# Optimization experiments

Hardware: AMD Instinct MI355X
Metric: run time of the kernel (lower is better)

The kernel has to match this reference:

```python
import jax, jax.numpy as jnp
import numpy as np

L, C, H, DH, S, N, B = 12, 768, 12, 64, 2, 577, 1
ALT_START, ROPE_START = 0, 0
OUT_LAYERS = (2, 5, 8, 11)
EPS = 1e-6


def _ln(x, w, b):
    m = jnp.mean(x, axis=-1, keepdims=True)
    v = jnp.var(x, axis=-1, keepdims=True)
    return (x - m) * jax.lax.rsqrt(v + EPS) * w + b


def _rms(x, w):
    return x * jax.lax.rsqrt(jnp.mean(x * x, axis=-1, keepdims=True) + EPS) * w


def _rot_half(x):
    h = x.shape[-1] // 2
    return jnp.concatenate([-x[..., h:], x[..., :h]], axis=-1)


def _rope(t, cos, sin):
    # t: [Bf, H, N, DH]; cos/sin: [N, DH] split into y/x halves
    h = t.shape[-1] // 2
    tv, th = t[..., :h], t[..., h:]
    cy, cx = cos[..., :h], cos[..., h:]
    sy, sx = sin[..., :h], sin[..., h:]
    return jnp.concatenate([tv * cy + _rot_half(tv) * sy,
                            th * cx + _rot_half(th) * sx], axis=-1)


def _block(xf, cos, sin, kv, p):
    (qkv_w, qkv_b, qn, kn, pw, pb, g1, g2,
     n1w, n1b, n2w, n2b, f1w, f1b, f2w, f2b) = p
    Bf, Nn, Cc = xf.shape
    h = _ln(xf, n1w, n1b)
    qkv = (jnp.einsum('bnc,oc->bno', h, qkv_w) + qkv_b)
    qkv = qkv.reshape(Bf, Nn, 3, H, DH).transpose(2, 0, 3, 1, 4)
    q, k, v = qkv[0], qkv[1], qkv[2]
    q, k = _rms(q, qn), _rms(k, kn)
    q, k = _rope(q, cos, sin), _rope(k, cos, sin)
    bias = ((1.0 - kv) * (-10000.0))[:, None, None, :]
    scores = jnp.einsum('bhqd,bhkd->bhqk', q, k) / np.sqrt(DH) + bias
    attn = jax.nn.softmax(scores, axis=-1)
    o = jnp.einsum('bhqk,bhkd->bhqd', attn, v).transpose(0, 2, 1, 3).reshape(Bf, Nn, Cc)
    o = jnp.einsum('bnc,oc->bno', o, pw) + pb
    xf = xf + g1 * o
    h2 = _ln(xf, n2w, n2b)
    m = jax.nn.gelu(jnp.einsum('bnc,oc->bno', h2, f1w) + f1b, approximate=False)
    m = jnp.einsum('bnd,od->bno', m, f2w) + f2b
    return xf + g2 * m


def _forward(x, rope_cos_local, rope_sin_local, rope_cos_global, rope_sin_global,
             key_valid_local, key_valid_global, camera_token,
             qkv_w, qkv_b, q_norm_w, k_norm_w, proj_w, proj_b,
             ls1_gamma, ls2_gamma, norm1_w, norm1_b, norm2_w, norm2_b,
             fc1_w, fc1_b, fc2_w, fc2_b, final_norm_w, final_norm_b):
    Bb, Ss, Nn, Cc = x.shape
    stacked = (qkv_w, qkv_b, q_norm_w, k_norm_w, proj_w, proj_b, ls1_gamma,
               ls2_gamma, norm1_w, norm1_b, norm2_w, norm2_b, fc1_w, fc1_b,
               fc2_w, fc2_b)
    local_x = x
    outputs = []
    cam_token_out = None
    max_out = max(OUT_LAYERS)
    for i in range(L):
        if i == ALT_START:
            ref = jnp.broadcast_to(camera_token[:, :1], (Bb, 1, Cc))
            src = jnp.broadcast_to(camera_token[:, 1:], (Bb, Ss - 1, Cc))
            x = x.at[:, :, 0].set(jnp.concatenate([ref, src], axis=1))
        p = tuple(a[i] for a in stacked)
        is_global = (i % 2 == 1)  # alt_start == 0
        if is_global:
            xf = x.reshape(Bb, Ss * Nn, Cc)
            xf = _block(xf, rope_cos_global, rope_sin_global, key_valid_global, p)
            x = xf.reshape(Bb, Ss, Nn, Cc)
        else:
            xf = x.reshape(Bb * Ss, Nn, Cc)
            xf = _block(xf, rope_cos_local, rope_sin_local, key_valid_local, p)
            x = xf.reshape(Bb, Ss, Nn, Cc)
            local_x = x
        if i in OUT_LAYERS:
            out_x = jnp.concatenate([local_x, x], axis=-1)  # cat_token=True
            outputs.append(out_x)
            if i == max_out:
                cam_token_out = out_x[:, :, 0]
    processed = []
    for o in outputs:
        o = jnp.concatenate([o[..., :Cc], _ln(o[..., Cc:], final_norm_w, final_norm_b)], axis=-1)
        o = o[..., 1:, :]  # drop cam/cls token (num_register_tokens=0)
        processed.append(o)
    return (processed[0], processed[1], processed[2], processed[3], cam_token_out)


def setup_inputs() -> dict:
    key = jax.random.key(0)
    ks = iter(jax.random.split(key, 40))
    rn = lambda sh, s=0.02: jax.random.normal(next(ks), sh, dtype=jnp.float32) * s
    two_pi = 2.0 * np.pi
    ang_l = jax.random.uniform(next(ks), (N, DH), dtype=jnp.float32) * two_pi
    ang_g = jax.random.uniform(next(ks), (S * N, DH), dtype=jnp.float32) * two_pi
    kv_l = (jax.random.uniform(next(ks), (B * S, N)) > 0.1).astype(jnp.float32)
    kv_g = (jax.random.uniform(next(ks), (B, S * N)) > 0.1).astype(jnp.float32)
    return {
        'x': rn((B, S, N, C), 1.0),
        'rope_cos_local': jnp.cos(ang_l), 'rope_sin_local': jnp.sin(ang_l),
        'rope_cos_global': jnp.cos(ang_g), 'rope_sin_global': jnp.sin(ang_g),
        'key_valid_local': kv_l, 'key_valid_global': kv_g,
        'camera_token': rn((1, 2, C)),
        'qkv_w': rn((L, 3 * C, C)), 'qkv_b': rn((L, 3 * C)),
        'q_norm_w': jnp.ones((L, DH), jnp.float32),
        'k_norm_w': jnp.ones((L, DH), jnp.float32),
        'proj_w': rn((L, C, C)), 'proj_b': rn((L, C)),
        'ls1_gamma': rn((L, C), 0.1), 'ls2_gamma': rn((L, C), 0.1),
        'norm1_w': jnp.ones((L, C), jnp.float32), 'norm1_b': jnp.zeros((L, C), jnp.float32),
        'norm2_w': jnp.ones((L, C), jnp.float32), 'norm2_b': jnp.zeros((L, C), jnp.float32),
        'fc1_w': rn((L, 4 * C, C)), 'fc1_b': rn((L, 4 * C)),
        'fc2_w': rn((L, C, 4 * C)), 'fc2_b': rn((L, C)),
        'final_norm_w': jnp.ones((C,), jnp.float32),
        'final_norm_b': jnp.zeros((C,), jnp.float32),
    }


def reference(x, rope_cos_local, rope_sin_local, rope_cos_global, rope_sin_global,
              key_valid_local, key_valid_global, camera_token,
              qkv_w, qkv_b, q_norm_w, k_norm_w, proj_w, proj_b,
              ls1_gamma, ls2_gamma, norm1_w, norm1_b, norm2_w, norm2_b,
              fc1_w, fc1_b, fc2_w, fc2_b, final_norm_w, final_norm_b):
    return _forward(x, rope_cos_local, rope_sin_local, rope_cos_global, rope_sin_global,
                    key_valid_local, key_valid_global, camera_token,
                    qkv_w, qkv_b, q_norm_w, k_norm_w, proj_w, proj_b,
                    ls1_gamma, ls2_gamma, norm1_w, norm1_b, norm2_w, norm2_b,
                    fc1_w, fc1_b, fc2_w, fc2_b, final_norm_w, final_norm_b)
```

## Files before the change

### kernel.cpp

```cpp
#include <hip/hip_runtime.h>
#include <hip/hip_bf16.h>
#include <math.h>

typedef __hip_bfloat16 bf16;
typedef __attribute__((ext_vector_type(4))) float floatx4;
typedef __attribute__((ext_vector_type(8))) short shortx8;

#define T_TOK 1154
#define C_DIM 768
#define H_HEADS 12
#define NLOC 577
#define OUT_PER 1769472

#define NQ  1769472ull
#define NP  589824ull
#define NF1 2359296ull
#define NF2 2359296ull
#define NWTOT 7077888ull
#define WQ  0ull
#define WP  1769472ull
#define WF1 2359296ull
#define WF2 4718592ull

static __device__ __forceinline__ float b2f(bf16 v) { return __bfloat162float(v); }
static __device__ __forceinline__ bf16 f2b(float v) { return __float2bfloat16(v); }

__global__ void k_init(const float* __restrict__ xin, const float* __restrict__ cam,
                       float* __restrict__ xF, int total) {
    int idx = blockIdx.x * 256 + threadIdx.x;
    if (idx >= total) return;
    int t = idx / C_DIM, c = idx - t * C_DIM;
    int s = t / NLOC, n = t - s * NLOC;
    float v = (n == 0) ? cam[s * C_DIM + c] : xin[idx];
    xF[idx] = v;
}

__global__ void k_cast(const float* __restrict__ src, bf16* __restrict__ dst, int total) {
    int idx = blockIdx.x * 256 + threadIdx.x;
    if (idx < total) dst[idx] = f2b(src[idx]);
}

__global__ __launch_bounds__(256) void k_wconv(
    const float* __restrict__ wq, const float* __restrict__ wp,
    const float* __restrict__ wf1, const float* __restrict__ wf2,
    bf16* __restrict__ dst) {
    size_t e = ((size_t)blockIdx.x * 256 + threadIdx.x) * 8;
    if (e >= NWTOT) return;
    const float* src; size_t off;
    if (e < WP)       { src = wq;  off = e; }
    else if (e < WF1) { src = wp;  off = e - WP; }
    else if (e < WF2) { src = wf1; off = e - WF1; }
    else              { src = wf2; off = e - WF2; }
    float4 a = *(const float4*)(src + off);
    float4 b = *(const float4*)(src + off + 4);
    bf16 pk[8];
    pk[0] = f2b(a.x); pk[1] = f2b(a.y); pk[2] = f2b(a.z); pk[3] = f2b(a.w);
    pk[4] = f2b(b.x); pk[5] = f2b(b.y); pk[6] = f2b(b.z); pk[7] = f2b(b.w);
    *(shortx8*)(dst + e) = *(shortx8*)pk;
}

__global__ __launch_bounds__(256) void k_ln(const float* __restrict__ xF,
                                            const float* __restrict__ w, const float* __restrict__ b,
                                            bf16* __restrict__ out) {
    int t = blockIdx.x;
    const float* xr = xF + (size_t)t * C_DIM;
    float s = 0.f, s2 = 0.f;
    for (int c = threadIdx.x; c < C_DIM; c += 256) { float v = xr[c]; s += v; s2 += v * v; }
    __shared__ float red[8];
    for (int o = 32; o; o >>= 1) { s += __shfl_xor(s, o, 64); s2 += __shfl_xor(s2, o, 64); }
    int wv = threadIdx.x >> 6;
    if ((threadIdx.x & 63) == 0) { red[wv] = s; red[4 + wv] = s2; }
    __syncthreads();
    s = red[0] + red[1] + red[2] + red[3];
    s2 = red[4] + red[5] + red[6] + red[7];
    float mean = s * (1.0f / C_DIM);
    float var = s2 * (1.0f / C_DIM) - mean * mean;
    if (var < 0.f) var = 0.f;
    float inv = rsqrtf(var + 1e-6f);
    bf16* orow = out + (size_t)t * C_DIM;
    for (int c = threadIdx.x; c < C_DIM; c += 256) {
        float v = (xr[c] - mean) * inv * w[c] + b[c];
        orow[c] = f2b(v);
    }
}

__global__ __launch_bounds__(256) void k_gemm(
    const bf16* __restrict__ A, const bf16* __restrict__ Bt,
    const float* __restrict__ bias, const float* __restrict__ gamma,
    bf16* __restrict__ outB, float* __restrict__ xio,
    int M, int N, int K, int mB, int mode) {
    __shared__ short At[64 * 72];
    __shared__ short Bs[64 * 72];
    int nwg = gridDim.x;
    int lid = blockIdx.x;
    int qd = nwg >> 3, rm = nwg & 7;
    int xcd = lid & 7, pos = lid >> 3;
    int lid2 = (xcd < rm ? xcd * (qd + 1) : rm * (qd + 1) + (xcd - rm) * qd) + pos;
    int mI = lid2 % mB, nI = lid2 / mB;
    int m0 = mI * 64, n0 = nI * 64;
    int tid = threadIdx.x;
    int wv = tid >> 6, lane = tid & 63;
    int mt = (wv & 1) * 32, nt = (wv >> 1) * 32;
    floatx4 acc[2][2] = {};
    int r = tid >> 2, cS = (tid & 3) * 16;
    int arow = m0 + r; if (arow >= M) arow = M - 1;
    const bf16* aptr = A + (size_t)arow * K + cS;
    const bf16* bptr = Bt + (size_t)(n0 + r) * K + cS;
    short* asl = &At[r * 72 + cS];
    short* bsl = &Bs[r * 72 + cS];
    int lrow = lane & 15, lq = lane >> 4;
    const short* aRd = &At[(mt + lrow) * 72 + lq * 8];
    const short* bRd = &Bs[(nt + lrow) * 72 + lq * 8];
    for (int k0 = 0; k0 < K; k0 += 64) {
        *(uint4*)asl       = *(const uint4*)(aptr);
        *(uint4*)(asl + 8) = *(const uint4*)(aptr + 8);
        *(uint4*)bsl       = *(const uint4*)(bptr);
        *(uint4*)(bsl + 8) = *(const uint4*)(bptr + 8);
        aptr += 64; bptr += 64;
        __syncthreads();
        shortx8 a00 = *(const shortx8*)(aRd);
        shortx8 a10 = *(const shortx8*)(aRd + 16 * 72);
        shortx8 b00 = *(const shortx8*)(bRd);
        shortx8 b10 = *(const shortx8*)(bRd + 16 * 72);
        shortx8 a01 = *(const shortx8*)(aRd + 32);
        shortx8 a11 = *(const shortx8*)(aRd + 16 * 72 + 32);
        shortx8 b01 = *(const shortx8*)(bRd + 32);
        shortx8 b11 = *(const shortx8*)(bRd + 16 * 72 + 32);
        acc[0][0] = __builtin_amdgcn_mfma_f32_16x16x32_bf16(a00, b00, acc[0][0], 0, 0, 0);
        acc[0][1] = __builtin_amdgcn_mfma_f32_16x16x32_bf16(a00, b10, acc[0][1], 0, 0, 0);
        acc[1][0] = __builtin_amdgcn_mfma_f32_16x16x32_bf16(a10, b00, acc[1][0], 0, 0, 0);
        acc[1][1] = __builtin_amdgcn_mfma_f32_16x16x32_bf16(a10, b10, acc[1][1], 0, 0, 0);
        acc[0][0] = __builtin_amdgcn_mfma_f32_16x16x32_bf16(a01, b01, acc[0][0], 0, 0, 0);
        acc[0][1] = __builtin_amdgcn_mfma_f32_16x16x32_bf16(a01, b11, acc[0][1], 0, 0, 0);
        acc[1][0] = __builtin_amdgcn_mfma_f32_16x16x32_bf16(a11, b01, acc[1][0], 0, 0, 0);
        acc[1][1] = __builtin_amdgcn_mfma_f32_16x16x32_bf16(a11, b11, acc[1][1], 0, 0, 0);
        __syncthreads();
    }
    int colb = n0 + nt + lrow;
    for (int mi = 0; mi < 2; mi++) {
        for (int ni = 0; ni < 2; ni++) {
            int cc = colb + ni * 16;
            #pragma unroll
            for (int rg = 0; rg < 4; rg++) {
                int rr = m0 + mt + mi * 16 + lq * 4 + rg;
                if (rr < M) {
                    float u = acc[mi][ni][rg] + bias[cc];
                    if (mode == 1) {
                        float g = 0.5f * u * (1.0f + erff(u * 0.70710678118f));
                        outB[(size_t)rr * N + cc] = f2b(g);
                    } else if (mode == 2) {
                        xio[(size_t)rr * N + cc] += gamma[cc] * u;
                    } else {
                        outB[(size_t)rr * N + cc] = f2b(u);
                    }
                }
            }
        }
    }
}

__global__ __launch_bounds__(256) void k_qkprep(
    const bf16* __restrict__ qkv,
    const float* __restrict__ qnw, const float* __restrict__ knw,
    const float* __restrict__ ctab, const float* __restrict__ stab, int posMod,
    bf16* __restrict__ qh, bf16* __restrict__ kh, bf16* __restrict__ vh) {
    int gw = blockIdx.x * 4 + (threadIdx.x >> 6);
    int lane = threadIdx.x & 63;
    if (gw >= T_TOK * H_HEADS) return;
    int t = gw / H_HEADS, h = gw - t * H_HEADS;
    size_t base = (size_t)t * 2304 + h * 64 + lane;
    float q = b2f(qkv[base]), k = b2f(qkv[base + 768]), v = b2f(qkv[base + 1536]);
    float sq = q * q, sk = k * k;
    for (int o = 32; o; o >>= 1) { sq += __shfl_xor(sq, o, 64); sk += __shfl_xor(sk, o, 64); }
    q = q * rsqrtf(sq * (1.0f / 64.0f) + 1e-6f) * qnw[lane];
    k = k * rsqrtf(sk * (1.0f / 64.0f) + 1e-6f) * knw[lane];
    int pos = t % posMod;
    float cv = ctab[pos * 64 + lane];
    float sv = stab[pos * 64 + lane];
    float qp = __shfl_xor(q, 16, 64);
    float kp = __shfl_xor(k, 16, 64);
    float sgn = (lane & 16) ? 1.0f : -1.0f;
    float qo = q * cv + sgn * qp * sv;
    float ko = k * cv + sgn * kp * sv;
    size_t oidx = ((size_t)h * T_TOK + t) * 64 + lane;
    qh[oidx] = f2b(qo);
    kh[oidx] = f2b(ko);
    vh[oidx] = f2b(v);
}

__global__ __launch_bounds__(256) void k_attn2(
    const bf16* __restrict__ qh, const bf16* __restrict__ kh, const bf16* __restrict__ vh,
    const float* __restrict__ mask, bf16* __restrict__ out, int nk) {
    __shared__ short Ks[64 * 72];
    __shared__ short Vs[64 * 72];
    __shared__ short Ps[4][16 * 72];
    __shared__ float bias_s[64];
    int h = blockIdx.y;
    int base = blockIdx.z * nk;
    int tid = threadIdx.x;
    int wv = tid >> 6, lane = tid & 63;
    int lr = lane & 15, lq = lane >> 4;
    int q0 = blockIdx.x * 64 + wv * 16;
    shortx8 qf[2];
    {
        int qr = q0 + lr; if (qr >= nk) qr = nk - 1;
        const bf16* qp = qh + ((size_t)h * T_TOK + base + qr) * 64 + lq * 8;
        qf[0] = *(const shortx8*)(qp);
        qf[1] = *(const shortx8*)(qp + 32);
    }
    float mrow[4] = {-3.0e38f, -3.0e38f, -3.0e38f, -3.0e38f};
    float lrow[4] = {0.f, 0.f, 0.f, 0.f};
    floatx4 accO[4] = {};
    short* pbuf = &Ps[wv][0];
    int nkt = (nk + 63) >> 6;
    for (int kt0 = 0; kt0 < nkt; kt0++) {
        int kbase = kt0 * 64;
        __syncthreads();
        for (int idx = tid; idx < 64 * 8; idx += 256) {
            int kr = idx >> 3, seg = idx & 7;
            int gk = kbase + kr;
            shortx8 v = {};
            if (gk < nk) v = *(const shortx8*)(kh + ((size_t)h * T_TOK + base + gk) * 64 + seg * 8);
            *(shortx8*)&Ks[kr * 72 + seg * 8] = v;
        }
        for (int idx = tid; idx < 64 * 8; idx += 256) {
            int kr = idx & 63, seg = idx >> 6;
            int gk = kbase + kr;
            shortx8 v = {};
            if (gk < nk) v = *(const shortx8*)(vh + ((size_t)h * T_TOK + base + gk) * 64 + seg * 8);
            bf16* vb = (bf16*)&v;
            #pragma unroll
            for (int j = 0; j < 8; j++)
                Vs[(seg * 8 + j) * 72 + kr] = *(short*)&vb[j];
        }
        if (tid < 64) {
            int gk = kbase + tid;
            bias_s[tid] = (gk < nk) ? (1.0f - mask[base + gk]) * -10000.0f : -30000.0f;
        }
        __syncthreads();
        floatx4 s[4];
        #pragma unroll
        for (int nt = 0; nt < 4; nt++) {
            floatx4 accS = {};
            shortx8 k0 = *(const shortx8*)&Ks[(nt * 16 + lr) * 72 + lq * 8];
            shortx8 k1 = *(const shortx8*)&Ks[(nt * 16 + lr) * 72 + 32 + lq * 8];
            accS = __builtin_amdgcn_mfma_f32_16x16x32_bf16(qf[0], k0, accS, 0, 0, 0);
            accS = __builtin_amdgcn_mfma_f32_16x16x32_bf16(qf[1], k1, accS, 0, 0, 0);
            s[nt] = accS;
        }
        float tmax[4] = {-3.0e38f, -3.0e38f, -3.0e38f, -3.0e38f};
        #pragma unroll
        for (int nt = 0; nt < 4; nt++) {
            float bv = bias_s[nt * 16 + lr];
            #pragma unroll
            for (int rg = 0; rg < 4; rg++) {
                float sv = s[nt][rg] * 0.125f + bv;
                s[nt][rg] = sv;
                tmax[rg] = fmaxf(tmax[rg], sv);
            }
        }
        #pragma unroll
        for (int rg = 0; rg < 4; rg++) {
            for (int o = 1; o < 16; o <<= 1) tmax[rg] = fmaxf(tmax[rg], __shfl_xor(tmax[rg], o, 16));
        }
        float fac[4], tsum[4] = {0.f, 0.f, 0.f, 0.f};
        #pragma unroll
        for (int rg = 0; rg < 4; rg++) {
            float mn = fmaxf(mrow[rg], tmax[rg]);
            fac[rg] = __expf(mrow[rg] - mn);
            mrow[rg] = mn;
        }
        #pragma unroll
        for (int nt = 0; nt < 4; nt++) {
            #pragma unroll
            for (int rg = 0; rg < 4; rg++) {
                float e = __expf(s[nt][rg] - mrow[rg]);
                s[nt][rg] = e;
                tsum[rg] += e;
            }
        }
        #pragma unroll
        for (int rg = 0; rg < 4; rg++) {
            for (int o = 1; o < 16; o <<= 1) tsum[rg] += __shfl_xor(tsum[rg], o, 16);
            lrow[rg] = lrow[rg] * fac[rg] + tsum[rg];
        }
        #pragma unroll
        for (int dt = 0; dt < 4; dt++)
            #pragma unroll
            for (int rg = 0; rg < 4; rg++) accO[dt][rg] *= fac[rg];
        #pragma unroll
        for (int nt = 0; nt < 4; nt++) {
            #pragma unroll
            for (int rg = 0; rg < 4; rg++) {
                bf16 pv = f2b(s[nt][rg]);
                pbuf[(lq * 4 + rg) * 72 + nt * 16 + lr] = *(short*)&pv;
            }
        }
        #pragma unroll
        for (int ks = 0; ks < 2; ks++) {
            shortx8 pf = *(const shortx8*)&pbuf[lr * 72 + ks * 32 + lq * 8];
            #pragma unroll
            for (int dt = 0; dt < 4; dt++) {
                shortx8 vf = *(const shortx8*)&Vs[(dt * 16 + lr) * 72 + ks * 32 + lq * 8];
                accO[dt] = __builtin_amdgcn_mfma_f32_16x16x32_bf16(pf, vf, accO[dt], 0, 0, 0);
            }
        }
    }
    float invl[4];
    #pragma unroll
    for (int rg = 0; rg < 4; rg++) invl[rg] = 1.0f / lrow[rg];
    #pragma unroll
    for (int rg = 0; rg < 4; rg++) {
        int qr = q0 + lq * 4 + rg;
        if (qr < nk) {
            bf16* orow = out + (size_t)(base + qr) * C_DIM + h * 64 + lr;
            #pragma unroll
            for (int dt = 0; dt < 4; dt++)
                orow[dt * 16] = f2b(accO[dt][rg] * invl[rg]);
        }
    }
}

__global__ __launch_bounds__(256) void k_output(
    const float* __restrict__ xF, const bf16* __restrict__ lxB,
    const float* __restrict__ fw, const float* __restrict__ fb, float* __restrict__ dst) {
    int b = blockIdx.x;
    int s = b / 576, nn = b - s * 576;
    int t = s * NLOC + nn + 1;
    const float* xr = xF + (size_t)t * C_DIM;
    float sum = 0.f, s2 = 0.f;
    for (int c = threadIdx.x; c < C_DIM; c += 256) { float v = xr[c]; sum += v; s2 += v * v; }
    __shared__ float red[8];
    for (int o = 32; o; o >>= 1) { sum += __shfl_xor(sum, o, 64); s2 += __shfl_xor(s2, o, 64); }
    if ((threadIdx.x & 63) == 0) { red[threadIdx.x >> 6] = sum; red[4 + (threadIdx.x >> 6)] = s2; }
    __syncthreads();
    sum = red[0] + red[1] + red[2] + red[3];
    s2 = red[4] + red[5] + red[6] + red[7];
    float mean = sum * (1.0f / C_DIM);
    float var = s2 * (1.0f / C_DIM) - mean * mean;
    if (var < 0.f) var = 0.f;
    float inv = rsqrtf(var + 1e-6f);
    float* orow = dst + (size_t)b * 1536;
    const bf16* lr = lxB + (size_t)t * C_DIM;
    for (int c = threadIdx.x; c < C_DIM; c += 256) {
        orow[c] = b2f(lr[c]);
        float v = (xr[c] - mean) * inv * fw[c] + fb[c];
        orow[768 + c] = v;
    }
}

__global__ void k_cam(const float* __restrict__ xF, const bf16* __restrict__ lxB,
                      float* __restrict__ dst) {
    for (int idx = threadIdx.x; idx < 2 * 1536; idx += 256) {
        int s = idx / 1536, c = idx - s * 1536;
        int t = s * NLOC;
        float v = (c < 768) ? b2f(lxB[(size_t)t * 768 + c]) : xF[(size_t)t * 768 + (c - 768)];
        dst[idx] = v;
    }
}

extern "C" void kernel_launch(void* const* d_in, const int* in_sizes, int n_in,
                              void* d_out, int out_size, void* d_ws, size_t ws_size,
                              hipStream_t stream) {
    const float* xin  = (const float*)d_in[0];
    const float* rcl  = (const float*)d_in[1];
    const float* rsl  = (const float*)d_in[2];
    const float* rcg  = (const float*)d_in[3];
    const float* rsg  = (const float*)d_in[4];
    const float* kvl  = (const float*)d_in[5];
    const float* kvg  = (const float*)d_in[6];
    const float* cam  = (const float*)d_in[7];
    const float* qkvw = (const float*)d_in[8];
    const float* qkvb = (const float*)d_in[9];
    const float* qnw  = (const float*)d_in[10];
    const float* knw  = (const float*)d_in[11];
    const float* pw   = (const float*)d_in[12];
    const float* pb   = (const float*)d_in[13];
    const float* ls1  = (const float*)d_in[14];
    const float* ls2  = (const float*)d_in[15];
    const float* n1w  = (const float*)d_in[16];
    const float* n1b  = (const float*)d_in[17];
    const float* n2w  = (const float*)d_in[18];
    const float* n2b  = (const float*)d_in[19];
    const float* f1w  = (const float*)d_in[20];
    const float* f1b  = (const float*)d_in[21];
    const float* f2w  = (const float*)d_in[22];
    const float* f2b_ = (const float*)d_in[23];
    const float* fnw  = (const float*)d_in[24];
    const float* fnb  = (const float*)d_in[25];

    char* ws = (char*)d_ws;
    const size_t TC = (size_t)T_TOK * C_DIM;
    float* xF  = (float*)ws; ws += TC * 4;
    bf16* bufA = (bf16*)ws;  ws += (size_t)T_TOK * 3072 * 2;
    bf16* qhb  = (bf16*)ws;  ws += TC * 2;
    bf16* khb  = (bf16*)ws;  ws += TC * 2;
    bf16* vhb  = (bf16*)ws;  ws += TC * 2;
    bf16* hbuf = (bf16*)ws;  ws += TC * 2;
    bf16* lxB  = (bf16*)ws;  ws += TC * 2;
    bf16* wB   = (bf16*)ws;  ws += NWTOT * 2;
    (void)ws_size; (void)n_in; (void)in_sizes; (void)out_size;

    float* out_b = (float*)d_out;

    k_init<<<(int)((TC + 255) / 256), 256, 0, stream>>>(xin, cam, xF, (int)TC);

    int outIdx = 0;
    for (int i = 0; i < 12; i++) {
        bool isGlobal = (i & 1);
        k_wconv<<<3456, 256, 0, stream>>>(
            qkvw + (size_t)i * NQ, pw + (size_t)i * NP,
            f1w + (size_t)i * NF1, f2w + (size_t)i * NF2, wB);
        k_ln<<<T_TOK, 256, 0, stream>>>(xF, n1w + (size_t)i * 768, n1b + (size_t)i * 768, hbuf);
        k_gemm<<<19 * 36, 256, 0, stream>>>(hbuf, wB + WQ,
            qkvb + (size_t)i * 2304, nullptr, bufA, nullptr, T_TOK, 2304, 768, 19, 3);
        k_qkprep<<<(T_TOK * H_HEADS) / 4, 256, 0, stream>>>(bufA,
            qnw + (size_t)i * 64, knw + (size_t)i * 64,
            isGlobal ? rcg : rcl, isGlobal ? rsg : rsl, isGlobal ? 1154 : 577,
            qhb, khb, vhb);
        if (isGlobal)
            k_attn2<<<dim3(19, 12, 1), 256, 0, stream>>>(qhb, khb, vhb, kvg, hbuf, 1154);
        else
            k_attn2<<<dim3(10, 12, 2), 256, 0, stream>>>(qhb, khb, vhb, kvl, hbuf, 577);
        k_gemm<<<19 * 12, 256, 0, stream>>>(hbuf, wB + WP,
            pb + (size_t)i * 768, ls1 + (size_t)i * 768, nullptr, xF, T_TOK, 768, 768, 19, 2);
        k_ln<<<T_TOK, 256, 0, stream>>>(xF, n2w + (size_t)i * 768, n2b + (size_t)i * 768, hbuf);
        k_gemm<<<19 * 48, 256, 0, stream>>>(hbuf, wB + WF1,
            f1b + (size_t)i * 3072, nullptr, bufA, nullptr, T_TOK, 3072, 768, 19, 1);
        k_gemm<<<19 * 12, 256, 0, stream>>>(bufA, wB + WF2,
            f2b_ + (size_t)i * 768, ls2 + (size_t)i * 768, nullptr, xF, T_TOK, 768, 3072, 19, 2);

        if (i == 2 || i == 4 || i == 8 || i == 10)
            k_cast<<<(int)((TC + 255) / 256), 256, 0, stream>>>(xF, lxB, (int)TC);

        if (i == 2 || i == 5 || i == 8 || i == 11) {
            k_output<<<1152, 256, 0, stream>>>(xF, lxB, fnw, fnb, out_b + (size_t)outIdx * OUT_PER);
            if (i == 11)
                k_cam<<<1, 256, 0, stream>>>(xF, lxB, out_b + 4ull * OUT_PER);
            outIdx++;
        }
    }
}
```

Baseline: 2.168 ms.

## Template GEMM with LDS-direct double buffering, larger tiles, split-K, hoisted weight conversion

```diff
diff --git a/kernel.cpp b/kernel.cpp
--- a/kernel.cpp
+++ b/kernel.cpp
@@ -25,6 +25,12 @@
 static __device__ __forceinline__ float b2f(bf16 v) { return __bfloat162float(v); }
 static __device__ __forceinline__ bf16 f2b(float v) { return __float2bfloat16(v); }
 
+static __device__ __forceinline__ void gload16(const bf16* g, short* l) {
+    __builtin_amdgcn_global_load_lds(
+        (__attribute__((address_space(1))) void*)(void*)g,
+        (__attribute__((address_space(3))) void*)(void*)l, 16, 0, 0);
+}
+
 __global__ void k_init(const float* __restrict__ xin, const float* __restrict__ cam,
                        float* __restrict__ xF, int total) {
     int idx = blockIdx.x * 256 + threadIdx.x;
@@ -40,19 +46,20 @@
     if (idx < total) dst[idx] = f2b(src[idx]);
 }
 
-__global__ __launch_bounds__(256) void k_wconv(
+__global__ __launch_bounds__(256) void k_wconv_all(
     const float* __restrict__ wq, const float* __restrict__ wp,
     const float* __restrict__ wf1, const float* __restrict__ wf2,
-    bf16* __restrict__ dst) {
+    bf16* __restrict__ dst, int nL) {
     size_t e = ((size_t)blockIdx.x * 256 + threadIdx.x) * 8;
-    if (e >= NWTOT) return;
-    const float* src; size_t off;
-    if (e < WP)       { src = wq;  off = e; }
-    else if (e < WF1) { src = wp;  off = e - WP; }
-    else if (e < WF2) { src = wf1; off = e - WF1; }
-    else              { src = wf2; off = e - WF2; }
-    float4 a = *(const float4*)(src + off);
-    float4 b = *(const float4*)(src + off + 4);
+    if (e >= (size_t)nL * NWTOT) return;
+    size_t layer = e / NWTOT, off = e - layer * NWTOT;
+    const float* src; size_t o2;
+    if (off < WP)       { src = wq  + layer * NQ;  o2 = off; }
+    else if (off < WF1) { src = wp  + layer * NP;  o2 = off - WP; }
+    else if (off < WF2) { src = wf1 + layer * NF1; o2 = off - WF1; }
+    else                { src = wf2 + layer * NF2; o2 = off - WF2; }
+    float4 a = *(const float4*)(src + o2);
+    float4 b = *(const float4*)(src + o2 + 4);
     bf16 pk[8];
     pk[0] = f2b(a.x); pk[1] = f2b(a.y); pk[2] = f2b(a.z); pk[3] = f2b(a.w);
     pk[4] = f2b(b.x); pk[5] = f2b(b.y); pk[6] = f2b(b.z); pk[7] = f2b(b.w);
@@ -84,73 +91,95 @@
     }
 }
 
-__global__ __launch_bounds__(256) void k_gemm(
+template<int BM, int BN, int MODE>
+__global__ __launch_bounds__(256) void k_gemmT(
     const bf16* __restrict__ A, const bf16* __restrict__ Bt,
     const float* __restrict__ bias, const float* __restrict__ gamma,
     bf16* __restrict__ outB, float* __restrict__ xio,
-    int M, int N, int K, int mB, int mode) {
-    __shared__ short At[64 * 72];
-    __shared__ short Bs[64 * 72];
+    int M, int N, int K, int mB, int kS) {
+    constexpr int FM = BM / 32;
+    constexpr int FN = BN / 32;
+    __shared__ short At[2][BM * 32];
+    __shared__ short Bs[2][BN * 32];
     int nwg = gridDim.x;
     int lid = blockIdx.x;
     int qd = nwg >> 3, rm = nwg & 7;
     int xcd = lid & 7, pos = lid >> 3;
     int lid2 = (xcd < rm ? xcd * (qd + 1) : rm * (qd + 1) + (xcd - rm) * qd) + pos;
-    int mI = lid2 % mB, nI = lid2 / mB;
-    int m0 = mI * 64, n0 = nI * 64;
+    int mI = lid2 % mB;
+    int rest = lid2 / mB;
+    int nB = N / BN;
+    int nI = rest % nB;
+    int kI = rest / nB;
+    int m0 = mI * BM, n0 = nI * BN;
+    int Ksub = K / kS;
+    int kOff = kI * Ksub;
     int tid = threadIdx.x;
-    int wv = tid >> 6, lane = tid & 63;
-    int mt = (wv & 1) * 32, nt = (wv >> 1) * 32;
-    floatx4 acc[2][2] = {};
-    int r = tid >> 2, cS = (tid & 3) * 16;
-    int arow = m0 + r; if (arow >= M) arow = M - 1;
-    const bf16* aptr = A + (size_t)arow * K + cS;
-    const bf16* bptr = Bt + (size_t)(n0 + r) * K + cS;
-    short* asl = &At[r * 72 + cS];
-    short* bsl = &Bs[r * 72 + cS];
-    int lrow = lane & 15, lq = lane >> 4;
-    const short* aRd = &At[(mt + lrow) * 72 + lq * 8];
-    const short* bRd = &Bs[(nt + lrow) * 72 + lq * 8];
-    for (int k0 = 0; k0 < K; k0 += 64) {
-        *(uint4*)asl       = *(const uint4*)(aptr);
-        *(uint4*)(asl + 8) = *(const uint4*)(aptr + 8);
-        *(uint4*)bsl       = *(const uint4*)(bptr);
-        *(uint4*)(bsl + 8) = *(const uint4*)(bptr + 8);
-        aptr += 64; bptr += 64;
+    int w = tid >> 6, lane = tid & 63;
+    int lr = lane & 15, lq = lane >> 4;
+    int wm = w & 1, wn = w >> 1;
+    int srow = lane >> 2, schk = lane & 3;
+    floatx4 acc[FM][FN] = {};
+
+    auto stage = [&](int buf, int k0) {
+        #pragma unroll
+        for (int j = 0; j < BM / 64; j++) {
+            int ia = w * (BM / 64) + j;
+            int row = ia * 16 + srow;
+            int ar = m0 + row; if (ar >= M) ar = M - 1;
+            gload16(A + (size_t)ar * K + kOff + k0 + schk * 8, &At[buf][ia * 512]);
+        }
+        #pragma unroll
+        for (int j = 0; j < BN / 64; j++) {
+            int ib = w * (BN / 64) + j;
+            int row = ib * 16 + srow;
+            gload16(Bt + (size_t)(n0 + row) * K + kOff + k0 + schk * 8, &Bs[buf][ib * 512]);
+        }
+    };
+
+    int nt = Ksub / 32;
+    stage(0, 0);
+    __syncthreads();
+    int cur = 0;
+    for (int t = 0; t < nt; ++t) {
+        if (t + 1 < nt) stage(cur ^ 1, (t + 1) * 32);
+        const short* aRd = &At[cur][(wm * (BM / 2) + lr) * 32 + lq * 8];
+        const short* bRd = &Bs[cur][(wn * (BN / 2) + lr) * 32 + lq * 8];
+        shortx8 af[FM], bg[FN];
+        #pragma unroll
+        for (int mi = 0; mi < FM; mi++) af[mi] = *(const shortx8*)(aRd + mi * 512);
+        #pragma unroll
+        for (int ni = 0; ni < FN; ni++) bg[ni] = *(const shortx8*)(bRd + ni * 512);
+        #pragma unroll
+        for (int mi = 0; mi < FM; mi++)
+            #pragma unroll
+            for (int ni = 0; ni < FN; ni++)
+                acc[mi][ni] = __builtin_amdgcn_mfma_f32_16x16x32_bf16(af[mi], bg[ni], acc[mi][ni], 0, 0, 0);
         __syncthreads();
-        shortx8 a00 = *(const shortx8*)(aRd);
-        shortx8 a10 = *(const shortx8*)(aRd + 16 * 72);
-        shortx8 b00 = *(const shortx8*)(bRd);
-        shortx8 b10 = *(const shortx8*)(bRd + 16 * 72);
-        shortx8 a01 = *(const shortx8*)(aRd + 32);
-        shortx8 a11 = *(const shortx8*)(aRd + 16 * 72 + 32);
-        shortx8 b01 = *(const shortx8*)(bRd + 32);
-        shortx8 b11 = *(const shortx8*)(bRd + 16 * 72 + 32);
-        acc[0][0] = __builtin_amdgcn_mfma_f32_16x16x32_bf16(a00, b00, acc[0][0], 0, 0, 0);
-        acc[0][1] = __builtin_amdgcn_mfma_f32_16x16x32_bf16(a00, b10, acc[0][1], 0, 0, 0);
-        acc[1][0] = __builtin_amdgcn_mfma_f32_16x16x32_bf16(a10, b00, acc[1][0], 0, 0, 0);
-        acc[1][1] = __builtin_amdgcn_mfma_f32_16x16x32_bf16(a10, b10, acc[1][1], 0, 0, 0);
-        acc[0][0] = __builtin_amdgcn_mfma_f32_16x16x32_bf16(a01, b01, acc[0][0], 0, 0, 0);
-        acc[0][1] = __builtin_amdgcn_mfma_f32_16x16x32_bf16(a01, b11, acc[0][1], 0, 0, 0);
-        acc[1][0] = __builtin_amdgcn_mfma_f32_16x16x32_bf16(a11, b01, acc[1][0], 0, 0, 0);
-        acc[1][1] = __builtin_amdgcn_mfma_f32_16x16x32_bf16(a11, b11, acc[1][1], 0, 0, 0);
-        __syncthreads();
-    }
-    int colb = n0 + nt + lrow;
-    for (int mi = 0; mi < 2; mi++) {
-        for (int ni = 0; ni < 2; ni++) {
-            int cc = colb + ni * 16;
+        cur ^= 1;
+    }
+
+    #pragma unroll
+    for (int mi = 0; mi < FM; mi++) {
+        #pragma unroll
+        for (int ni = 0; ni < FN; ni++) {
+            int cc = n0 + wn * (BN / 2) + ni * 16 + lr;
             #pragma unroll
             for (int rg = 0; rg < 4; rg++) {
-                int rr = m0 + mt + mi * 16 + lq * 4 + rg;
+                int rr = m0 + wm * (BM / 2) + mi * 16 + lq * 4 + rg;
                 if (rr < M) {
-                    float u = acc[mi][ni][rg] + bias[cc];
-                    if (mode == 1) {
+                    float u = acc[mi][ni][rg];
+                    if (MODE == 2) {
+                        u += (kI == 0) ? bias[cc] : 0.f;
+                        float contrib = gamma[cc] * u;
+                        if (kS > 1) atomicAdd(&xio[(size_t)rr * N + cc], contrib);
+                        else        xio[(size_t)rr * N + cc] += contrib;
+                    } else if (MODE == 1) {
+                        u += bias[cc];
                         float g = 0.5f * u * (1.0f + erff(u * 0.70710678118f));
                         outB[(size_t)rr * N + cc] = f2b(g);
-                    } else if (mode == 2) {
-                        xio[(size_t)rr * N + cc] += gamma[cc] * u;
                     } else {
+                        u += bias[cc];
                         outB[(size_t)rr * N + cc] = f2b(u);
                     }
                 }
@@ -398,22 +427,32 @@
     bf16* vhb  = (bf16*)ws;  ws += TC * 2;
     bf16* hbuf = (bf16*)ws;  ws += TC * 2;
     bf16* lxB  = (bf16*)ws;  ws += TC * 2;
-    bf16* wB   = (bf16*)ws;  ws += NWTOT * 2;
-    (void)ws_size; (void)n_in; (void)in_sizes; (void)out_size;
+    bf16* wAll = (bf16*)ws;
+    size_t usedBase = (size_t)(ws - (char*)d_ws);
+    bool bigW = ws_size >= usedBase + 12ull * NWTOT * 2ull;
+    (void)n_in; (void)in_sizes; (void)out_size;
 
     float* out_b = (float*)d_out;
 
     k_init<<<(int)((TC + 255) / 256), 256, 0, stream>>>(xin, cam, xF, (int)TC);
+    if (bigW)
+        k_wconv_all<<<41472, 256, 0, stream>>>(qkvw, pw, f1w, f2w, wAll, 12);
 
     int outIdx = 0;
     for (int i = 0; i < 12; i++) {
         bool isGlobal = (i & 1);
-        k_wconv<<<3456, 256, 0, stream>>>(
-            qkvw + (size_t)i * NQ, pw + (size_t)i * NP,
-            f1w + (size_t)i * NF1, f2w + (size_t)i * NF2, wB);
+        bf16* wL;
+        if (bigW) {
+            wL = wAll + (size_t)i * NWTOT;
+        } else {
+            k_wconv_all<<<3456, 256, 0, stream>>>(
+                qkvw + (size_t)i * NQ, pw + (size_t)i * NP,
+                f1w + (size_t)i * NF1, f2w + (size_t)i * NF2, wAll, 1);
+            wL = wAll;
+        }
         k_ln<<<T_TOK, 256, 0, stream>>>(xF, n1w + (size_t)i * 768, n1b + (size_t)i * 768, hbuf);
-        k_gemm<<<19 * 36, 256, 0, stream>>>(hbuf, wB + WQ,
-            qkvb + (size_t)i * 2304, nullptr, bufA, nullptr, T_TOK, 2304, 768, 19, 3);
+        k_gemmT<128, 128, 3><<<180, 256, 0, stream>>>(hbuf, wL + WQ,
+            qkvb + (size_t)i * 2304, nullptr, bufA, nullptr, T_TOK, 2304, 768, 10, 1);
         k_qkprep<<<(T_TOK * H_HEADS) / 4, 256, 0, stream>>>(bufA,
             qnw + (size_t)i * 64, knw + (size_t)i * 64,
             isGlobal ? rcg : rcl, isGlobal ? rsg : rsl, isGlobal ? 1154 : 577,
@@ -422,13 +461,13 @@
             k_attn2<<<dim3(19, 12, 1), 256, 0, stream>>>(qhb, khb, vhb, kvg, hbuf, 1154);
         else
             k_attn2<<<dim3(10, 12, 2), 256, 0, stream>>>(qhb, khb, vhb, kvl, hbuf, 577);
-        k_gemm<<<19 * 12, 256, 0, stream>>>(hbuf, wB + WP,
+        k_gemmT<64, 64, 2><<<456, 256, 0, stream>>>(hbuf, wL + WP,
             pb + (size_t)i * 768, ls1 + (size_t)i * 768, nullptr, xF, T_TOK, 768, 768, 19, 2);
         k_ln<<<T_TOK, 256, 0, stream>>>(xF, n2w + (size_t)i * 768, n2b + (size_t)i * 768, hbuf);
-        k_gemm<<<19 * 48, 256, 0, stream>>>(hbuf, wB + WF1,
-            f1b + (size_t)i * 3072, nullptr, bufA, nullptr, T_TOK, 3072, 768, 19, 1);
-        k_gemm<<<19 * 12, 256, 0, stream>>>(bufA, wB + WF2,
-            f2b_ + (size_t)i * 768, ls2 + (size_t)i * 768, nullptr, xF, T_TOK, 768, 3072, 19, 2);
+        k_gemmT<128, 128, 1><<<240, 256, 0, stream>>>(hbuf, wL + WF1,
+            f1b + (size_t)i * 3072, nullptr, bufA, nullptr, T_TOK, 3072, 768, 10, 1);
+        k_gemmT<64, 64, 2><<<912, 256, 0, stream>>>(bufA, wL + WF2,
+            f2b_ + (size_t)i * 768, ls2 + (size_t)i * 768, nullptr, xF, T_TOK, 768, 3072, 19, 4);
 
         if (i == 2 || i == 4 || i == 8 || i == 10)
             k_cast<<<(int)((TC + 255) / 256), 256, 0, stream>>>(xF, lxB, (int)TC);
```

Result: slower. 2.314 ms (+6.7%).
